# Kernel optimization log

Hardware: AMD Instinct MI355X
Metric: run time of the kernel (lower is better)

## Reference

```python
import jax, jax.numpy as jnp
import numpy as np

N = 100000
E = 800000
D = 128


def setup_inputs() -> dict:
    key = jax.random.key(0)
    k1, k2, k3, k4 = jax.random.split(key, 4)
    x = jax.random.normal(k1, (N, D), dtype=jnp.float32)
    edge_index = jax.random.randint(k2, (2, E), 0, N, dtype=jnp.int64)
    s = 1.0 / np.sqrt(D)
    W1 = jax.random.uniform(k3, (D, D), jnp.float32, -s, s)
    b1 = jnp.zeros((D,), jnp.float32)
    W2 = jax.random.uniform(k4, (D, D), jnp.float32, -s, s)
    b2 = jnp.zeros((D,), jnp.float32)
    return {"x": x, "edge_index": edge_index, "W1": W1, "b1": b1, "W2": W2, "b2": b2}


def _degree(idx, n, dtype):
    return jax.ops.segment_sum(jnp.ones(idx.shape, dtype), idx, num_segments=n)


def _graph_conv(x, row, col, W, b, residual, act):
    n = x.shape[0]
    deg_out = jnp.clip(_degree(row, n, x.dtype), 1.0)          # [N]
    x_src = x * jax.lax.rsqrt(deg_out)[:, None]                # [N, D]
    # scatter-add messages from source (row) into target (col)
    agg = jax.ops.segment_sum(x_src[row], col, num_segments=n)  # [N, D]
    out = agg @ W.T + b
    deg_in = jnp.clip(_degree(col, n, x.dtype), 1.0)
    out = out * jax.lax.rsqrt(deg_in)[:, None]
    if residual:
        out = out + x  # res_fc is Identity (in_dim == out_dim)
    if act:
        out = jax.nn.relu(out)
    return out


def reference(x, edge_index, W1, b1, W2, b2):
    row, col = edge_index[0], edge_index[1]
    # layer 1: relu + residual; layer 2 (last, encoding=False): no act, no residual
    h = _graph_conv(x, row, col, W1, b1, residual=True, act=True)
    h = _graph_conv(h, row, col, W2, b2, residual=False, act=False)
    return h
```

## Files before the change

kernel.cpp:

```cpp
#include <hip/hip_runtime.h>


#define NN 100000
#define EE 800000
#define DD 128
#define NB1 98
#define NTILE (NN / 16)
#define NXCD 8

typedef __attribute__((ext_vector_type(8))) short short8;
typedef __attribute__((ext_vector_type(4))) float floatx4;

__device__ inline float bf2f(unsigned int u16) {
    union { unsigned int i; float f; } c;
    c.i = u16 << 16;
    return c.f;
}
__device__ inline ushort f2bf(float f) {
    union { float f; unsigned int i; } c;
    c.f = f;
    unsigned int u = c.i;
    return (ushort)((u + 0x7fffu + ((u >> 16) & 1u)) >> 16);
}

__device__ inline unsigned int xcc_id() {
    unsigned int x;
    asm volatile("s_getreg_b32 %0, hwreg(HW_REG_XCC_ID)" : "=s"(x));
    return x & (NXCD - 1);
}

__global__ __launch_bounds__(256) void count_kernel(const int* __restrict__ row,
                                                    const int* __restrict__ col,
                                                    int* __restrict__ partial_out,
                                                    int* __restrict__ partial_in,
                                                    int* __restrict__ off) {
    int e = blockIdx.x * 256 + threadIdx.x;
    if (e < EE) {
        unsigned int k = xcc_id();
        int c = col[e];
        int slot = __hip_atomic_fetch_add(&partial_in[k * NN + c], 1,
                                          __ATOMIC_RELAXED, __HIP_MEMORY_SCOPE_WORKGROUP);
        off[e] = slot | (int)(k << 28);
        __hip_atomic_fetch_add(&partial_out[k * NN + row[e]], 1,
                               __ATOMIC_RELAXED, __HIP_MEMORY_SCOPE_WORKGROUP);
    }
}

__global__ __launch_bounds__(256) void node_kernel(const int* __restrict__ partial_out,
                                                   const int* __restrict__ partial_in,
                                                   int* __restrict__ cnt_total,
                                                   int* __restrict__ xoff,
                                                   float* __restrict__ dinv_out,
                                                   float* __restrict__ dinv_in) {
    int n = blockIdx.x * 256 + threadIdx.x;
    if (n >= NN) return;
    int din = 0, dout = 0;
#pragma unroll
    for (int k = 0; k < NXCD; ++k) {
        int v = partial_in[k * NN + n];
        xoff[k * NN + n] = din;
        din += v;
        dout += partial_out[k * NN + n];
    }
    cnt_total[n] = din;
    dinv_in[n]  = rsqrtf((float)max(din, 1));
    dinv_out[n] = rsqrtf((float)max(dout, 1));
}

__global__ __launch_bounds__(256) void scan1_kernel(const int* __restrict__ cnt,
                                                    int* __restrict__ excl,
                                                    int* __restrict__ bsums) {
    __shared__ int tmp[256];
    const int t = threadIdx.x;
    const int base = blockIdx.x * 1024 + t * 4;
    int a[4];
#pragma unroll
    for (int q = 0; q < 4; ++q) a[q] = (base + q < NN) ? cnt[base + q] : 0;
    int s = a[0] + a[1] + a[2] + a[3];
    tmp[t] = s;
    __syncthreads();
    for (int off = 1; off < 256; off <<= 1) {
        int v = 0;
        if (t >= off) v = tmp[t - off];
        __syncthreads();
        tmp[t] += v;
        __syncthreads();
    }
    int excl_s = tmp[t] - s;
    if (t == 255) bsums[blockIdx.x] = tmp[t];
    int run = excl_s;
#pragma unroll
    for (int q = 0; q < 4; ++q) {
        if (base + q < NN) excl[base + q] = run;
        run += a[q];
    }
}

__global__ __launch_bounds__(256) void scan2_kernel(int* __restrict__ bsums, int nb) {
    __shared__ int tmp[256];
    const int t = threadIdx.x;
    int s = (t < nb) ? bsums[t] : 0;
    tmp[t] = s;
    __syncthreads();
    for (int off = 1; off < 256; off <<= 1) {
        int v = 0;
        if (t >= off) v = tmp[t - off];
        __syncthreads();
        tmp[t] += v;
        __syncthreads();
    }
    if (t < nb) bsums[t] = tmp[t] - s;
}

__global__ __launch_bounds__(256) void scan3_kernel(const int* __restrict__ excl,
                                                    const int* __restrict__ bsums,
                                                    int* __restrict__ row_start) {
    int i = blockIdx.x * 256 + threadIdx.x;
    if (i < NN) row_start[i] = excl[i] + bsums[i >> 10];
}

__global__ __launch_bounds__(256) void fill_kernel(const int* __restrict__ row,
                                                   const int* __restrict__ col,
                                                   const int* __restrict__ row_start,
                                                   const int* __restrict__ xoff,
                                                   const int* __restrict__ off,
                                                   int* __restrict__ srcs) {
    int e = blockIdx.x * 256 + threadIdx.x;
    if (e < EE) {
        int c = col[e];
        unsigned int o = (unsigned int)off[e];
        int k = (int)(o >> 28);
        int slot = (int)(o & 0x0FFFFFFFu);
        srcs[row_start[c] + xoff[k * NN + c] + slot] = row[e];
    }
}

__global__ __launch_bounds__(256) void prescale_kernel(const float* __restrict__ x,
                                                       const float* __restrict__ dinv_out,
                                                       ushort* __restrict__ xb) {
    int idx = blockIdx.x * 256 + threadIdx.x;
    if (idx >= NN * 32) return;
    int n = idx >> 5;
    float s = dinv_out[n];
    float4 v = ((const float4*)x)[idx];
    ushort4 o;
    o.x = f2bf(v.x * s);
    o.y = f2bf(v.y * s);
    o.z = f2bf(v.z * s);
    o.w = f2bf(v.w * s);
    ((ushort4*)xb)[idx] = o;
}

__global__ __launch_bounds__(256) void gather_kernel(const ushort* __restrict__ src,
                                                     const int* __restrict__ row_start,
                                                     const int* __restrict__ srcs,
                                                     ushort* __restrict__ agg) {
    const int node = blockIdx.x * 16 + (threadIdx.x >> 4);
    const int lane = threadIdx.x & 15;
    if (node >= NN) return;
    int p = row_start[node];
    const int end = (node + 1 < NN) ? row_start[node + 1] : EE;
    float a0 = 0.f, a1 = 0.f, a2 = 0.f, a3 = 0.f;
    float a4 = 0.f, a5 = 0.f, a6 = 0.f, a7 = 0.f;

#define ACCUM(V)                                     \
    do {                                             \
        a0 += bf2f((V).x & 0xffffu);                 \
        a1 += bf2f((V).x >> 16);                     \
        a2 += bf2f((V).y & 0xffffu);                 \
        a3 += bf2f((V).y >> 16);                     \
        a4 += bf2f((V).z & 0xffffu);                 \
        a5 += bf2f((V).z >> 16);                     \
        a6 += bf2f((V).w & 0xffffu);                 \
        a7 += bf2f((V).w >> 16);                     \
    } while (0)

    for (; p + 3 < end; p += 4) {
        int s0 = srcs[p];
        int s1 = srcs[p + 1];
        int s2 = srcs[p + 2];
        int s3 = srcs[p + 3];
        uint4 v0 = ((const uint4*)(src + (size_t)s0 * DD))[lane];
        uint4 v1 = ((const uint4*)(src + (size_t)s1 * DD))[lane];
        uint4 v2 = ((const uint4*)(src + (size_t)s2 * DD))[lane];
        uint4 v3 = ((const uint4*)(src + (size_t)s3 * DD))[lane];
        ACCUM(v0); ACCUM(v1); ACCUM(v2); ACCUM(v3);
    }
    for (; p < end; ++p) {
        int s0 = srcs[p];
        uint4 v0 = ((const uint4*)(src + (size_t)s0 * DD))[lane];
        ACCUM(v0);
    }
#undef ACCUM

    uint4 o;
    o.x = (unsigned int)f2bf(a0) | ((unsigned int)f2bf(a1) << 16);
    o.y = (unsigned int)f2bf(a2) | ((unsigned int)f2bf(a3) << 16);
    o.z = (unsigned int)f2bf(a4) | ((unsigned int)f2bf(a5) << 16);
    o.w = (unsigned int)f2bf(a6) | ((unsigned int)f2bf(a7) << 16);
    ((uint4*)(agg + (size_t)node * DD))[lane] = o;
}

template <bool L1>
__global__ __launch_bounds__(256) void gemm_ep(const ushort* __restrict__ agg,
                                               const float* __restrict__ W,
                                               const float* __restrict__ bias,
                                               const float* __restrict__ dinv_in,
                                               const float* __restrict__ dinv_out,
                                               const float* __restrict__ x,
                                               ushort* __restrict__ hs,
                                               float* __restrict__ out) {
    __shared__ ushort Ws[128 * 136];
    {
        int j = threadIdx.x >> 1;
        int k0 = (threadIdx.x & 1) * 64;
        const float4* wp = (const float4*)(W + (size_t)j * DD + k0);
        ushort* dst = Ws + j * 136 + k0;
#pragma unroll
        for (int q = 0; q < 16; ++q) {
            float4 v = wp[q];
            ushort4 o;
            o.x = f2bf(v.x); o.y = f2bf(v.y); o.z = f2bf(v.z); o.w = f2bf(v.w);
            *(ushort4*)(dst + q * 4) = o;
        }
    }
    __syncthreads();

    const int wave = threadIdx.x >> 6;
    const int lane = threadIdx.x & 63;
    const int tile = blockIdx.x * 4 + wave;
    if (tile >= NTILE) return;
    const int mi = lane & 15;
    const int quad = lane >> 4;
    const int m0 = tile * 16;

    floatx4 acc[8];
#pragma unroll
    for (int t = 0; t < 8; ++t) acc[t] = (floatx4){0.f, 0.f, 0.f, 0.f};

    const ushort* ap = agg + (size_t)(m0 + mi) * DD + quad * 8;
#pragma unroll
    for (int s = 0; s < 4; ++s) {
        short8 a = *(const short8*)(ap + s * 32);
#pragma unroll
        for (int t = 0; t < 8; ++t) {
            short8 b = *(const short8*)(Ws + (t * 16 + mi) * 136 + s * 32 + quad * 8);
            acc[t] = __builtin_amdgcn_mfma_f32_16x16x32_bf16(a, b, acc[t], 0, 0, 0);
        }
    }

    float dv[4], dov[4];
#pragma unroll
    for (int i = 0; i < 4; ++i) {
        int r = m0 + quad * 4 + i;
        dv[i] = dinv_in[r];
        if (L1) dov[i] = dinv_out[r];
    }
#pragma unroll
    for (int t = 0; t < 8; ++t) {
        int c = t * 16 + mi;
        float bv = bias[c];
#pragma unroll
        for (int i = 0; i < 4; ++i) {
            int r = m0 + quad * 4 + i;
            float o = (acc[t][i] + bv) * dv[i];
            if (L1) {
                o += x[(size_t)r * DD + c];
                o = fmaxf(o, 0.f);
                hs[(size_t)r * DD + c] = f2bf(o * dov[i]);
            } else {
                out[(size_t)r * DD + c] = o;
            }
        }
    }
}

extern "C" void kernel_launch(void* const* d_in, const int* in_sizes, int n_in,
                              void* d_out, int out_size, void* d_ws, size_t ws_size,
                              hipStream_t stream) {
    const float* x  = (const float*)d_in[0];
    const int*   ei = (const int*)d_in[1];
    const float* W1 = (const float*)d_in[2];
    const float* b1 = (const float*)d_in[3];
    const float* W2 = (const float*)d_in[4];
    const float* b2 = (const float*)d_in[5];
    float* out = (float*)d_out;

    const int* row = ei;
    const int* col = ei + EE;

    ushort* agg     = (ushort*)d_ws;
    ushort* xb      = agg + (size_t)NN * DD;
    float* dinv_out = (float*)(xb + (size_t)NN * DD);
    float* dinv_in  = dinv_out + NN;
    int*   cnt      = (int*)(dinv_in + NN);
    int*   excl     = cnt + 2 * NN;
    int*   row_st   = excl + NN;
    int*   srcs     = row_st + NN;
    int*   bsums    = srcs + EE;

    int* off         = (int*)agg;
    int* partial_in  = off + EE;
    int* partial_out = partial_in + NXCD * NN;
    int* xoff        = partial_out + NXCD * NN;

    hipMemsetAsync(partial_in, 0, (size_t)2 * NXCD * NN * sizeof(int), stream);
    count_kernel<<<(EE + 255) / 256, 256, 0, stream>>>(row, col, partial_out, partial_in, off);
    node_kernel<<<(NN + 255) / 256, 256, 0, stream>>>(partial_out, partial_in, cnt, xoff,
                                                      dinv_out, dinv_in);
    scan1_kernel<<<NB1, 256, 0, stream>>>(cnt, excl, bsums);
    scan2_kernel<<<1, 256, 0, stream>>>(bsums, NB1);
    scan3_kernel<<<(NN + 255) / 256, 256, 0, stream>>>(excl, bsums, row_st);
    fill_kernel<<<(EE + 255) / 256, 256, 0, stream>>>(row, col, row_st, xoff, off, srcs);

    prescale_kernel<<<(NN * 32 + 255) / 256, 256, 0, stream>>>(x, dinv_out, xb);
    gather_kernel<<<(NN + 15) / 16, 256, 0, stream>>>(xb, row_st, srcs, agg);
    gemm_ep<true><<<(NTILE + 3) / 4, 256, 0, stream>>>(agg, W1, b1, dinv_in, dinv_out, x,
                                                       xb, nullptr);

    gather_kernel<<<(NN + 15) / 16, 256, 0, stream>>>(xb, row_st, srcs, agg);
    gemm_ep<false><<<(NTILE + 3) / 4, 256, 0, stream>>>(agg, W2, b2, dinv_in, nullptr, nullptr,
                                                        nullptr, out);
}
```

Baseline: 319.6 us.

## Count degrees with LDS histograms per edge chunk and node range

Replaces the per-XCD global-atomic degree counting with a blocked histogram. Each of 200 blocks takes one of 8 edge chunks and one of 25 node ranges of 4096, counts in-degree and out-degree with LDS atomics, then writes its partial counts to global memory. This removes the memset and the contended global atomics. In exchange, every block reads its whole edge chunk (100k edges), so each edge is read 25 times, and the launch uses only 200 blocks.

```diff
diff --git a/kernel.cpp b/kernel.cpp
--- a/kernel.cpp
+++ b/kernel.cpp
@@ -6,7 +6,11 @@
 #define DD 128
 #define NB1 98
 #define NTILE (NN / 16)
-#define NXCD 8
+
+#define CC 8
+#define CH (EE / CC)
+#define RR 25
+#define NPR 4096
 
 typedef __attribute__((ext_vector_type(8))) short short8;
 typedef __attribute__((ext_vector_type(4))) float floatx4;
@@ -23,27 +27,34 @@
     return (ushort)((u + 0x7fffu + ((u >> 16) & 1u)) >> 16);
 }
 
-__device__ inline unsigned int xcc_id() {
-    unsigned int x;
-    asm volatile("s_getreg_b32 %0, hwreg(HW_REG_XCC_ID)" : "=s"(x));
-    return x & (NXCD - 1);
-}
-
-__global__ __launch_bounds__(256) void count_kernel(const int* __restrict__ row,
+__global__ __launch_bounds__(512) void count_kernel(const int* __restrict__ row,
                                                     const int* __restrict__ col,
                                                     int* __restrict__ partial_out,
                                                     int* __restrict__ partial_in,
                                                     int* __restrict__ off) {
-    int e = blockIdx.x * 256 + threadIdx.x;
-    if (e < EE) {
-        unsigned int k = xcc_id();
-        int c = col[e];
-        int slot = __hip_atomic_fetch_add(&partial_in[k * NN + c], 1,
-                                          __ATOMIC_RELAXED, __HIP_MEMORY_SCOPE_WORKGROUP);
-        off[e] = slot | (int)(k << 28);
-        __hip_atomic_fetch_add(&partial_out[k * NN + row[e]], 1,
-                               __ATOMIC_RELAXED, __HIP_MEMORY_SCOPE_WORKGROUP);
-    }
+    __shared__ int cin[NPR];
+    __shared__ int cout[NPR];
+    const int r = blockIdx.x % RR;
+    const int c = blockIdx.x / RR;
+    for (int i = threadIdx.x; i < NPR; i += 512) { cin[i] = 0; cout[i] = 0; }
+    __syncthreads();
+
+    const int base = c * CH;
+    for (int t = threadIdx.x; t < CH; t += 512) {
+        const int e = base + t;
+        const int cl = col[e];
+        const int rw = row[e];
+        if ((cl >> 12) == r) {
+            int slot = atomicAdd(&cin[cl & 4095], 1);
+            off[e] = slot | (c << 24);
+        }
+        if ((rw >> 12) == r) atomicAdd(&cout[rw & 4095], 1);
+    }
+    __syncthreads();
+
+    int* pin  = partial_in  + (c * RR + r) * NPR;
+    int* pout = partial_out + (c * RR + r) * NPR;
+    for (int i = threadIdx.x; i < NPR; i += 512) { pin[i] = cin[i]; pout[i] = cout[i]; }
 }
 
 __global__ __launch_bounds__(256) void node_kernel(const int* __restrict__ partial_out,
@@ -54,13 +65,15 @@
                                                    float* __restrict__ dinv_in) {
     int n = blockIdx.x * 256 + threadIdx.x;
     if (n >= NN) return;
+    const int r = n >> 12;
+    const int i = n & 4095;
     int din = 0, dout = 0;
 #pragma unroll
-    for (int k = 0; k < NXCD; ++k) {
-        int v = partial_in[k * NN + n];
-        xoff[k * NN + n] = din;
+    for (int c = 0; c < CC; ++c) {
+        int v = partial_in[(c * RR + r) * NPR + i];
+        xoff[c * NN + n] = din;
         din += v;
-        dout += partial_out[k * NN + n];
+        dout += partial_out[(c * RR + r) * NPR + i];
     }
     cnt_total[n] = din;
     dinv_in[n]  = rsqrtf((float)max(din, 1));
@@ -127,11 +140,11 @@
                                                    int* __restrict__ srcs) {
     int e = blockIdx.x * 256 + threadIdx.x;
     if (e < EE) {
-        int c = col[e];
-        unsigned int o = (unsigned int)off[e];
-        int k = (int)(o >> 28);
-        int slot = (int)(o & 0x0FFFFFFFu);
-        srcs[row_start[c] + xoff[k * NN + c] + slot] = row[e];
+        const int cl = col[e];
+        const unsigned int o = (unsigned int)off[e];
+        const int c = (int)(o >> 24);
+        const int slot = (int)(o & 0x00FFFFFFu);
+        srcs[row_start[cl] + xoff[c * NN + cl] + slot] = row[e];
     }
 }
 
@@ -301,11 +314,10 @@
 
     int* off         = (int*)agg;
     int* partial_in  = off + EE;
-    int* partial_out = partial_in + NXCD * NN;
-    int* xoff        = partial_out + NXCD * NN;
-
-    hipMemsetAsync(partial_in, 0, (size_t)2 * NXCD * NN * sizeof(int), stream);
-    count_kernel<<<(EE + 255) / 256, 256, 0, stream>>>(row, col, partial_out, partial_in, off);
+    int* partial_out = partial_in + CC * RR * NPR;
+    int* xoff        = partial_out + CC * RR * NPR;
+
+    count_kernel<<<CC * RR, 512, 0, stream>>>(row, col, partial_out, partial_in, off);
     node_kernel<<<(NN + 255) / 256, 256, 0, stream>>>(partial_out, partial_in, cnt, xoff,
                                                       dinv_out, dinv_in);
     scan1_kernel<<<NB1, 256, 0, stream>>>(cnt, excl, bsums);
```

New measurement: 344.9 us. 7.9% more time.
